# Optimization experiments

Measured on AMD Instinct MI355X. Metric: run time of the kernel, lower is better.

Reference implementation:

```python
import jax, jax.numpy as jnp
import numpy as np
from jax import lax

KERNEL_SIZE = 3
DIM = 64
FILTERS = 32
BATCH = 128
WIDTH = 8192
STRIDE = 1


def setup_inputs() -> dict:
    key = jax.random.key(0)
    k1, k2 = jax.random.split(key)
    x = jax.random.normal(k1, (BATCH, WIDTH, DIM), dtype=jnp.float32)
    # glorot-uniform init for the polar kernel, shape (kernel_size, dim, filters)
    fan_in = KERNEL_SIZE * DIM
    fan_out = KERNEL_SIZE * FILTERS
    limit = float(np.sqrt(6.0 / (fan_in + fan_out)))
    polar_kernel = jax.random.uniform(
        k2, (KERNEL_SIZE, DIM, FILTERS), dtype=jnp.float32,
        minval=-limit, maxval=limit)
    return {"x": x, "polar_kernel": polar_kernel}


def reference(x, polar_kernel):
    # Strided VALID 1D conv: (B, W, D) x (K, D, F) -> (B, W_out, F)
    out = lax.conv_general_dilated(
        x, polar_kernel,
        window_strides=(STRIDE,),
        padding="VALID",
        dimension_numbers=("NWC", "WIO", "NWC"))
    # expand to (B, W_out, F, 1); activation is identity (activation=None)
    out = out[..., None]
    # per-sample global min-max normalization over axes (1, 2, 3)
    mn = jnp.min(out, axis=(1, 2, 3), keepdims=True)
    mx = jnp.max(out, axis=(1, 2, 3), keepdims=True)
    return (out - mn) / (mx - mn)
```

## Files before the change

kernel.cpp:

```cpp
#include <hip/hip_runtime.h>
#include <hip/hip_bf16.h>

#define BATCH  128
#define WIDTH  8192
#define DIM    64
#define FILT   32
#define KSZ    3
#define WOUT   8190
#define RPW    14
#define RST    16
#define NW     8
#define WT     112
#define TPB    19
#define NBX    4
#define XROWS  (NW*RST + 2)

typedef __attribute__((ext_vector_type(8))) _Float16 f16x8;
typedef __attribute__((ext_vector_type(4))) float f32x4;
typedef __attribute__((ext_vector_type(4))) unsigned u32x4;

__global__ __launch_bounds__(512, 4)
void conv_min(const float* __restrict__ x, const float* __restrict__ ker,
              unsigned* __restrict__ c16, float* __restrict__ mm)
{
  __shared__ __align__(16) float xs[2][XROWS * DIM];
  __shared__ __align__(16) short ks[KSZ * FILT * DIM];
  __shared__ float red[2 * NW];

  const int t  = threadIdx.x;
  const int l  = t & 63;
  const int wv = t >> 6;
  const int b  = blockIdx.y;
  const int step0 = blockIdx.x * TPB;
  const float* xb = x + (long)b * WIDTH * DIM;

  auto stage = [&](int bb, int step) {
    long gw0 = (long)(step0 + step) * WT + wv * RPW;
    char* lb = (char*)&xs[bb][0] + wv * (RST * DIM * 4);
    #pragma unroll
    for (int j = 0; j < 4; ++j) {
      int row_l = j * 4 + (l >> 4);
      int slot  = (l & 15) ^ (row_l & 7);
      long gr = gw0 + row_l;
      if (gr > WIDTH - 1) gr = WIDTH - 1;
      __builtin_amdgcn_global_load_lds(
          (const __attribute__((address_space(1))) void*)(xb + gr * DIM + slot * 4),
          (__attribute__((address_space(3))) void*)(lb + j * 1024), 16, 0, 0);
    }
  };

  stage(0, 0);

  #pragma unroll
  for (int i = 0; i < 12; ++i) {
    int idx = t + i * 512;
    int k = idx >> 11, rem = idx & 2047;
    int d = rem >> 5,  f = rem & 31;
    _Float16 hv = (_Float16)ker[idx];
    int byte = ((k * FILT + f) * DIM + d) * 2;
    byte ^= (f & 7) << 4;
    ks[byte >> 1] = __builtin_bit_cast(short, hv);
  }
  __syncthreads();

  f16x8 Bf[KSZ][2][2];
  #pragma unroll
  for (int s = 0; s < KSZ; ++s)
    #pragma unroll
    for (int kh = 0; kh < 2; ++kh)
      #pragma unroll
      for (int nt = 0; nt < 2; ++nt) {
        int f  = 2 * (l & 15) + nt;
        int d0 = kh * 32 + (l >> 4) * 8;
        int byte = ((s * FILT + f) * DIM + d0) * 2;
        byte ^= (f & 7) << 4;
        Bf[s][kh][nt] = *reinterpret_cast<const f16x8*>(&ks[byte >> 1]);
      }

  float mx = -INFINITY, mn = INFINITY;

  int cur = 0;
  for (int it = 0; it < TPB; ++it) {
    if (it + 1 < TPB) {
      stage(cur ^ 1, it + 1);
      asm volatile("s_waitcnt vmcnt(8)" ::: "memory");
    } else {
      asm volatile("s_waitcnt vmcnt(4)" ::: "memory");
    }
    __builtin_amdgcn_sched_barrier(0);

    const float* xl = &xs[cur][0];
    f32x4 acc[2];
    acc[0] = (f32x4){0.f, 0.f, 0.f, 0.f};
    acc[1] = (f32x4){0.f, 0.f, 0.f, 0.f};

    #pragma unroll
    for (int s = 0; s < KSZ; ++s) {
      #pragma unroll
      for (int kh = 0; kh < 2; ++kh) {
        int ra = wv * RST + (l & 15) + s;
        int sg = kh * 8 + (l >> 4) * 2;
        int rb = ra & 7;
        f32x4 u0 = *reinterpret_cast<const f32x4*>(&xl[ra * DIM + ((sg    ) ^ rb) * 4]);
        f32x4 u1 = *reinterpret_cast<const f32x4*>(&xl[ra * DIM + ((sg + 1) ^ rb) * 4]);
        u32x4 pk;
        pk.x = __builtin_bit_cast(unsigned, __builtin_amdgcn_cvt_pkrtz(u0.x, u0.y));
        pk.y = __builtin_bit_cast(unsigned, __builtin_amdgcn_cvt_pkrtz(u0.z, u0.w));
        pk.z = __builtin_bit_cast(unsigned, __builtin_amdgcn_cvt_pkrtz(u1.x, u1.y));
        pk.w = __builtin_bit_cast(unsigned, __builtin_amdgcn_cvt_pkrtz(u1.z, u1.w));
        f16x8 av = __builtin_bit_cast(f16x8, pk);
        acc[0] = __builtin_amdgcn_mfma_f32_16x16x32_f16(av, Bf[s][kh][0], acc[0], 0, 0, 0);
        acc[1] = __builtin_amdgcn_mfma_f32_16x16x32_f16(av, Bf[s][kh][1], acc[1], 0, 0, 0);
      }
    }

    long gw0 = (long)(step0 + it) * WT + wv * RPW;
    #pragma unroll
    for (int r = 0; r < 4; ++r) {
      int wl = (l >> 4) * 4 + r;
      long gr = gw0 + wl;
      if (wl < RPW && gr < WOUT) {
        float v0 = acc[0][r];
        float v1 = acc[1][r];
        mx = fmaxf(mx, fmaxf(v0, v1));
        mn = fminf(mn, fminf(v0, v1));
        unsigned lo = __builtin_bit_cast(unsigned short, (_Float16)v0);
        unsigned hi = __builtin_bit_cast(unsigned short, (_Float16)v1);
        c16[((long)b * WOUT + gr) * 16 + (l & 15)] = lo | (hi << 16);
      }
    }
    cur ^= 1;
  }

  #pragma unroll
  for (int off = 32; off > 0; off >>= 1) {
    mx = fmaxf(mx, __shfl_down(mx, off));
    mn = fminf(mn, __shfl_down(mn, off));
  }
  if (l == 0) { red[wv * 2] = mx; red[wv * 2 + 1] = mn; }
  __syncthreads();
  if (t == 0) {
    float Mx = -INFINITY, Mn = INFINITY;
    #pragma unroll
    for (int w = 0; w < NW; ++w) {
      Mx = fmaxf(Mx, red[w * 2]);
      Mn = fminf(Mn, red[w * 2 + 1]);
    }
    mm[(b * NBX + blockIdx.x) * 2]     = Mx;
    mm[(b * NBX + blockIdx.x) * 2 + 1] = Mn;
  }
}

__global__ __launch_bounds__(256)
void norm_out(const unsigned* __restrict__ c16, const float* __restrict__ mm,
              float* __restrict__ out)
{
  const int b = blockIdx.y;
  float mx = -INFINITY, mn = INFINITY;
  #pragma unroll
  for (int i = 0; i < NBX; ++i) {
    mx = fmaxf(mx, mm[(b * NBX + i) * 2]);
    mn = fminf(mn, mm[(b * NBX + i) * 2 + 1]);
  }
  const float rs = 1.0f / (mx - mn);

  const int c = blockIdx.x * 256 + threadIdx.x;
  if (c < WOUT * 4) {
    u32x4 v = *reinterpret_cast<const u32x4*>(c16 + ((long)b * WOUT) * 16 + (long)c * 4);
    long base = (long)b * (WOUT * FILT) + (long)c * 8;
    f32x4 o0, o1;
    #pragma unroll
    for (int j = 0; j < 2; ++j) {
      unsigned u = v[j];
      o0[2*j]   = ((float)__builtin_bit_cast(_Float16, (unsigned short)(u & 0xffffu)) - mn) * rs;
      o0[2*j+1] = ((float)__builtin_bit_cast(_Float16, (unsigned short)(u >> 16))      - mn) * rs;
    }
    #pragma unroll
    for (int j = 0; j < 2; ++j) {
      unsigned u = v[2+j];
      o1[2*j]   = ((float)__builtin_bit_cast(_Float16, (unsigned short)(u & 0xffffu)) - mn) * rs;
      o1[2*j+1] = ((float)__builtin_bit_cast(_Float16, (unsigned short)(u >> 16))      - mn) * rs;
    }
    *reinterpret_cast<f32x4*>(out + base)     = o0;
    *reinterpret_cast<f32x4*>(out + base + 4) = o1;
  }
}

extern "C" void kernel_launch(void* const* d_in, const int* in_sizes, int n_in,
                              void* d_out, int out_size, void* d_ws, size_t ws_size,
                              hipStream_t stream) {
  const float* x   = (const float*)d_in[0];
  const float* ker = (const float*)d_in[1];
  float* out = (float*)d_out;
  float*    mm  = (float*)d_ws;
  unsigned* c16 = (unsigned*)((char*)d_ws + 4096);

  conv_min<<<dim3(NBX, BATCH), dim3(512), 0, stream>>>(x, ker, c16, mm);
  norm_out<<<dim3(128, BATCH), dim3(256), 0, stream>>>(c16, mm, out);
}
```

Before: 110.6 us.

## Fuse conv and normalization via per-batch atomic grid sync, holding results in registers

Merges the conv+minmax kernel and the normalization kernel into one. Each block keeps its fp16-packed outputs in registers, and the four blocks of a sample exchange min/max through atomics and a spin-wait. Each block then writes the normalized fp32 output directly. This removes the fp16 intermediate round-trip through global memory and one kernel launch. It also retiles to 16 rows per wave with full barriers each step and reads B fragments from LDS instead of registers. The spin-wait relies on all 512 blocks being co-resident, which is a deadlock risk, and the register hold array raises register pressure.

Measured after the change: 191.2 us. 1.73x slower.

```diff
diff --git a/kernel.cpp b/kernel.cpp
--- a/kernel.cpp
+++ b/kernel.cpp
@@ -7,36 +7,42 @@
 #define FILT   32
 #define KSZ    3
 #define WOUT   8190
-#define RPW    14
-#define RST    16
+
 #define NW     8
-#define WT     112
-#define TPB    19
+#define RPW    16
+#define WT     128
+#define TPB    16
 #define NBX    4
-#define XROWS  (NW*RST + 2)
+#define XR     130
 
 typedef __attribute__((ext_vector_type(8))) _Float16 f16x8;
 typedef __attribute__((ext_vector_type(4))) float f32x4;
 typedef __attribute__((ext_vector_type(4))) unsigned u32x4;
 
+__global__ void zero_cnt(unsigned* cnt) {
+  cnt[threadIdx.x] = 0u;
+}
+
 __global__ __launch_bounds__(512, 4)
-void conv_min(const float* __restrict__ x, const float* __restrict__ ker,
-              unsigned* __restrict__ c16, float* __restrict__ mm)
+void conv_norm(const float* __restrict__ x, const float* __restrict__ ker,
+               float* __restrict__ out, float* __restrict__ mm,
+               unsigned* __restrict__ cnt)
 {
-  __shared__ __align__(16) float xs[2][XROWS * DIM];
+  __shared__ __align__(16) float xs[2][XR * DIM];
   __shared__ __align__(16) short ks[KSZ * FILT * DIM];
   __shared__ float red[2 * NW];
 
   const int t  = threadIdx.x;
   const int l  = t & 63;
   const int wv = t >> 6;
-  const int b  = blockIdx.y;
-  const int step0 = blockIdx.x * TPB;
+  const int b  = blockIdx.x >> 2;
+  const int bx = blockIdx.x & 3;
+  const int step0 = bx * TPB;
   const float* xb = x + (long)b * WIDTH * DIM;
 
   auto stage = [&](int bb, int step) {
     long gw0 = (long)(step0 + step) * WT + wv * RPW;
-    char* lb = (char*)&xs[bb][0] + wv * (RST * DIM * 4);
+    char* lb = (char*)&xs[bb][0] + wv * (RPW * DIM * 4);
     #pragma unroll
     for (int j = 0; j < 4; ++j) {
       int row_l = j * 4 + (l >> 4);
@@ -47,6 +53,15 @@
           (const __attribute__((address_space(1))) void*)(xb + gr * DIM + slot * 4),
           (__attribute__((address_space(3))) void*)(lb + j * 1024), 16, 0, 0);
     }
+    if (wv == 7 && l < 32) {
+      int row_l = 16 + (l >> 4);
+      int slot  = (l & 15) ^ (row_l & 7);
+      long gr = gw0 + row_l;
+      if (gr > WIDTH - 1) gr = WIDTH - 1;
+      __builtin_amdgcn_global_load_lds(
+          (const __attribute__((address_space(1))) void*)(xb + gr * DIM + slot * 4),
+          (__attribute__((address_space(3))) void*)(lb + 4 * 1024), 16, 0, 0);
+    }
   };
 
   stage(0, 0);
@@ -58,47 +73,30 @@
     int d = rem >> 5,  f = rem & 31;
     _Float16 hv = (_Float16)ker[idx];
     int byte = ((k * FILT + f) * DIM + d) * 2;
-    byte ^= (f & 7) << 4;
+    byte ^= ((f >> 1) & 7) << 4;
     ks[byte >> 1] = __builtin_bit_cast(short, hv);
   }
   __syncthreads();
 
-  f16x8 Bf[KSZ][2][2];
-  #pragma unroll
-  for (int s = 0; s < KSZ; ++s)
-    #pragma unroll
-    for (int kh = 0; kh < 2; ++kh)
-      #pragma unroll
-      for (int nt = 0; nt < 2; ++nt) {
-        int f  = 2 * (l & 15) + nt;
-        int d0 = kh * 32 + (l >> 4) * 8;
-        int byte = ((s * FILT + f) * DIM + d0) * 2;
-        byte ^= (f & 7) << 4;
-        Bf[s][kh][nt] = *reinterpret_cast<const f16x8*>(&ks[byte >> 1]);
-      }
-
+  unsigned hold[TPB][4];
   float mx = -INFINITY, mn = INFINITY;
-
+  int kso = 0;
   int cur = 0;
+
+  #pragma unroll
   for (int it = 0; it < TPB; ++it) {
-    if (it + 1 < TPB) {
-      stage(cur ^ 1, it + 1);
-      asm volatile("s_waitcnt vmcnt(8)" ::: "memory");
-    } else {
-      asm volatile("s_waitcnt vmcnt(4)" ::: "memory");
-    }
-    __builtin_amdgcn_sched_barrier(0);
+    if (it + 1 < TPB) stage(cur ^ 1, it + 1);
+    asm volatile("" : "+v"(kso));
 
     const float* xl = &xs[cur][0];
-    f32x4 acc[2];
-    acc[0] = (f32x4){0.f, 0.f, 0.f, 0.f};
-    acc[1] = (f32x4){0.f, 0.f, 0.f, 0.f};
+    f32x4 acc0 = (f32x4){0.f, 0.f, 0.f, 0.f};
+    f32x4 acc1 = (f32x4){0.f, 0.f, 0.f, 0.f};
 
     #pragma unroll
     for (int s = 0; s < KSZ; ++s) {
       #pragma unroll
       for (int kh = 0; kh < 2; ++kh) {
-        int ra = wv * RST + (l & 15) + s;
+        int ra = wv * RPW + (l & 15) + s;
         int sg = kh * 8 + (l >> 4) * 2;
         int rb = ra & 7;
         f32x4 u0 = *reinterpret_cast<const f32x4*>(&xl[ra * DIM + ((sg    ) ^ rb) * 4]);
@@ -109,8 +107,18 @@
         pk.z = __builtin_bit_cast(unsigned, __builtin_amdgcn_cvt_pkrtz(u1.x, u1.y));
         pk.w = __builtin_bit_cast(unsigned, __builtin_amdgcn_cvt_pkrtz(u1.z, u1.w));
         f16x8 av = __builtin_bit_cast(f16x8, pk);
-        acc[0] = __builtin_amdgcn_mfma_f32_16x16x32_f16(av, Bf[s][kh][0], acc[0], 0, 0, 0);
-        acc[1] = __builtin_amdgcn_mfma_f32_16x16x32_f16(av, Bf[s][kh][1], acc[1], 0, 0, 0);
+
+        int d0 = kh * 32 + (l >> 4) * 8;
+        int f0 = 2 * (l & 15);
+        int byteA = ((s * FILT + f0) * DIM + d0) * 2;
+        byteA ^= ((f0 >> 1) & 7) << 4;
+        int byteB = ((s * FILT + f0 + 1) * DIM + d0) * 2;
+        byteB ^= (((f0 + 1) >> 1) & 7) << 4;
+        f16x8 B0 = *reinterpret_cast<const f16x8*>(&ks[(byteA >> 1) + kso]);
+        f16x8 B1 = *reinterpret_cast<const f16x8*>(&ks[(byteB >> 1) + kso]);
+
+        acc0 = __builtin_amdgcn_mfma_f32_16x16x32_f16(av, B0, acc0, 0, 0, 0);
+        acc1 = __builtin_amdgcn_mfma_f32_16x16x32_f16(av, B1, acc1, 0, 0, 0);
       }
     }
 
@@ -119,15 +127,18 @@
     for (int r = 0; r < 4; ++r) {
       int wl = (l >> 4) * 4 + r;
       long gr = gw0 + wl;
-      if (wl < RPW && gr < WOUT) {
-        float v0 = acc[0][r];
-        float v1 = acc[1][r];
+      float v0 = acc0[r], v1 = acc1[r];
+      if (gr < WOUT) {
         mx = fmaxf(mx, fmaxf(v0, v1));
         mn = fminf(mn, fminf(v0, v1));
-        unsigned lo = __builtin_bit_cast(unsigned short, (_Float16)v0);
-        unsigned hi = __builtin_bit_cast(unsigned short, (_Float16)v1);
-        c16[((long)b * WOUT + gr) * 16 + (l & 15)] = lo | (hi << 16);
       }
+      hold[it][r] = __builtin_bit_cast(unsigned, __builtin_amdgcn_cvt_pkrtz(v0, v1));
+    }
+
+    if (it + 1 < TPB) {
+      asm volatile("s_waitcnt vmcnt(0) lgkmcnt(0)" ::: "memory");
+      asm volatile("s_barrier" ::: "memory");
+      __builtin_amdgcn_sched_barrier(0);
     }
     cur ^= 1;
   }
@@ -146,43 +157,45 @@
       Mx = fmaxf(Mx, red[w * 2]);
       Mn = fminf(Mn, red[w * 2 + 1]);
     }
-    mm[(b * NBX + blockIdx.x) * 2]     = Mx;
-    mm[(b * NBX + blockIdx.x) * 2 + 1] = Mn;
-  }
-}
-
-__global__ __launch_bounds__(256)
-void norm_out(const unsigned* __restrict__ c16, const float* __restrict__ mm,
-              float* __restrict__ out)
-{
-  const int b = blockIdx.y;
-  float mx = -INFINITY, mn = INFINITY;
-  #pragma unroll
-  for (int i = 0; i < NBX; ++i) {
-    mx = fmaxf(mx, mm[(b * NBX + i) * 2]);
-    mn = fminf(mn, mm[(b * NBX + i) * 2 + 1]);
-  }
-  const float rs = 1.0f / (mx - mn);
-
-  const int c = blockIdx.x * 256 + threadIdx.x;
-  if (c < WOUT * 4) {
-    u32x4 v = *reinterpret_cast<const u32x4*>(c16 + ((long)b * WOUT) * 16 + (long)c * 4);
-    long base = (long)b * (WOUT * FILT) + (long)c * 8;
-    f32x4 o0, o1;
-    #pragma unroll
-    for (int j = 0; j < 2; ++j) {
-      unsigned u = v[j];
-      o0[2*j]   = ((float)__builtin_bit_cast(_Float16, (unsigned short)(u & 0xffffu)) - mn) * rs;
-      o0[2*j+1] = ((float)__builtin_bit_cast(_Float16, (unsigned short)(u >> 16))      - mn) * rs;
-    }
-    #pragma unroll
-    for (int j = 0; j < 2; ++j) {
-      unsigned u = v[2+j];
-      o1[2*j]   = ((float)__builtin_bit_cast(_Float16, (unsigned short)(u & 0xffffu)) - mn) * rs;
-      o1[2*j+1] = ((float)__builtin_bit_cast(_Float16, (unsigned short)(u >> 16))      - mn) * rs;
-    }
-    *reinterpret_cast<f32x4*>(out + base)     = o0;
-    *reinterpret_cast<f32x4*>(out + base + 4) = o1;
+    __hip_atomic_store(&mm[(b * NBX + bx) * 2],     Mx,
+                       __ATOMIC_RELEASE, __HIP_MEMORY_SCOPE_AGENT);
+    __hip_atomic_store(&mm[(b * NBX + bx) * 2 + 1], Mn,
+                       __ATOMIC_RELEASE, __HIP_MEMORY_SCOPE_AGENT);
+    __hip_atomic_fetch_add(&cnt[b], 1u, __ATOMIC_ACQ_REL, __HIP_MEMORY_SCOPE_AGENT);
+    while (__hip_atomic_load(&cnt[b], __ATOMIC_ACQUIRE, __HIP_MEMORY_SCOPE_AGENT) < 4u)
+      __builtin_amdgcn_s_sleep(2);
+    float GMx = -INFINITY, GMn = INFINITY;
+    #pragma unroll
+    for (int i = 0; i < NBX; ++i) {
+      GMx = fmaxf(GMx, __hip_atomic_load(&mm[(b * NBX + i) * 2],
+                                         __ATOMIC_ACQUIRE, __HIP_MEMORY_SCOPE_AGENT));
+      GMn = fminf(GMn, __hip_atomic_load(&mm[(b * NBX + i) * 2 + 1],
+                                         __ATOMIC_ACQUIRE, __HIP_MEMORY_SCOPE_AGENT));
+    }
+    red[0] = GMx; red[1] = GMn;
+  }
+  __syncthreads();
+
+  const float Mn = red[1];
+  const float rs = 1.0f / (red[0] - Mn);
+
+  #pragma unroll
+  for (int it = 0; it < TPB; ++it) {
+    long gw0 = (long)(step0 + it) * WT + wv * RPW;
+    #pragma unroll
+    for (int r = 0; r < 4; ++r) {
+      int wl = (l >> 4) * 4 + r;
+      long gr = gw0 + wl;
+      if (gr < WOUT) {
+        unsigned u = hold[it][r];
+        float v0 = (float)__builtin_bit_cast(_Float16, (unsigned short)(u & 0xffffu));
+        float v1 = (float)__builtin_bit_cast(_Float16, (unsigned short)(u >> 16));
+        float2 o;
+        o.x = (v0 - Mn) * rs;
+        o.y = (v1 - Mn) * rs;
+        *reinterpret_cast<float2*>(out + ((long)b * WOUT + gr) * FILT + 2 * (l & 15)) = o;
+      }
+    }
   }
 }
 
@@ -193,8 +206,8 @@
   const float* ker = (const float*)d_in[1];
   float* out = (float*)d_out;
   float*    mm  = (float*)d_ws;
-  unsigned* c16 = (unsigned*)((char*)d_ws + 4096);
-
-  conv_min<<<dim3(NBX, BATCH), dim3(512), 0, stream>>>(x, ker, c16, mm);
-  norm_out<<<dim3(128, BATCH), dim3(256), 0, stream>>>(c16, mm, out);
+  unsigned* cnt = (unsigned*)((char*)d_ws + 4096);
+
+  zero_cnt<<<dim3(1), dim3(128), 0, stream>>>(cnt);
+  conv_norm<<<dim3(NBX * BATCH), dim3(512), 0, stream>>>(x, ker, out, mm, cnt);
 }
```
